# Kernel tuning notes

Hardware: AMD Instinct MI355X
Metric: run time of the kernel (lower is better)

Reference implementation:

```python
import jax, jax.numpy as jnp
import numpy as np

HEAD_SIZE = 128
BLOCK_SIZE = 2048


def setup_inputs() -> dict:
    key = jax.random.key(0)
    k1, k2 = jax.random.split(key)
    B, T, D = 8, 2048, 1024
    x = jax.random.normal(k1, (B, T, D), dtype=jnp.float32)
    # Linear(dim, 3*head_size, bias=False): weight [3*head_size, dim], applied as x @ W.T
    W_qkv = jax.random.normal(k2, (3 * HEAD_SIZE, D), dtype=jnp.float32) * (1.0 / np.sqrt(D))
    return {"x": x, "W_qkv": W_qkv}


def reference(x, W_qkv):
    B, T, D = x.shape
    qkv = jnp.einsum('btd,hd->bth', x, W_qkv)  # [B, T, 3*head_size]
    q = qkv[:, :, :HEAD_SIZE]
    k = qkv[:, :, HEAD_SIZE:2 * HEAD_SIZE]
    v = qkv[:, :, 2 * HEAD_SIZE:]
    scale = 1.0 / np.sqrt(HEAD_SIZE).astype(np.float32)
    score = jnp.einsum('bqh,bkh->bqk', q, k) * scale  # [B, T, T]
    causal = jnp.tril(jnp.ones((T, T), dtype=bool))
    score = jnp.where(causal, score, -jnp.inf)
    attn = jax.nn.softmax(score, axis=-1)
    # dropout p=0.0 (eval) -> identity
    return jnp.einsum('bqk,bkh->bqh', attn, v)  # [B, T, head_size]
```

## Files before the change

### kernel.cpp

```cpp
#include <hip/hip_runtime.h>
#include <hip/hip_bf16.h>
#include <math.h>

#define D_MODEL 1024
#define TLEN    2048

typedef __attribute__((ext_vector_type(8))) short short8;
typedef __attribute__((ext_vector_type(4))) float f32x4;

static __device__ __forceinline__ unsigned short f2bf(float f) {
    __hip_bfloat16 h = __float2bfloat16(f);
    return __builtin_bit_cast(unsigned short, h);
}
static __device__ __forceinline__ float bf2f(unsigned short u) {
    unsigned int x = ((unsigned int)u) << 16;
    return __builtin_bit_cast(float, x);
}
static __device__ __forceinline__ void lds_cp16(void* lds, const void* g) {
    __builtin_amdgcn_global_load_lds(
        (const __attribute__((address_space(1))) unsigned int*)g,
        (__attribute__((address_space(3))) unsigned int*)lds, 16, 0, 0);
}

__global__ __launch_bounds__(256) void pack_w(const float* __restrict__ W,
                                              unsigned short* __restrict__ wt) {
    const int id = blockIdx.x * 256 + threadIdx.x;
    const int h  = id >> 7;
    const int kg = id & 127;
    const int k0 = kg * 8;
    const int kt = k0 >> 6;
    const int kin = k0 & 63;
    const int np = h >> 7;
    const int hp = h & 127;
    const float4 a = *(const float4*)&W[(size_t)h * D_MODEL + k0];
    const float4 b = *(const float4*)&W[(size_t)h * D_MODEL + k0 + 4];
    short8 v;
    v[0] = (short)f2bf(a.x); v[1] = (short)f2bf(a.y);
    v[2] = (short)f2bf(a.z); v[3] = (short)f2bf(a.w);
    v[4] = (short)f2bf(b.x); v[5] = (short)f2bf(b.y);
    v[6] = (short)f2bf(b.z); v[7] = (short)f2bf(b.w);
    const size_t dst = ((size_t)(np * 16 + kt) * 128 + hp) * 64 + (kin ^ ((hp & 7) * 8));
    *(short8*)&wt[dst] = v;
}

__global__ __launch_bounds__(256, 4) void qkv_gemm(const float* __restrict__ x,
                                                   const unsigned short* __restrict__ wt,
                                                   unsigned short* __restrict__ qk,
                                                   unsigned short* __restrict__ vt) {
    __shared__ unsigned short As[64][88];
    __shared__ unsigned short Bs[128 * 64];

    const int tid  = threadIdx.x;
    const int lane = tid & 63;
    const int w    = tid >> 6;
    const int wm   = w >> 1, wn = w & 1;
    const int cc   = lane & 15, g = lane >> 4;
    const int row0 = blockIdx.x * 64;
    const int np   = blockIdx.y;

    const int xr  = tid >> 2;
    const int xc0 = (tid & 3) * 16;

    const f32x4 zero = {0.f, 0.f, 0.f, 0.f};
    f32x4 acc[2][4];
#pragma unroll
    for (int i = 0; i < 2; ++i)
#pragma unroll
        for (int j = 0; j < 4; ++j) acc[i][j] = zero;

    const float* xrow = x + (size_t)(row0 + xr) * D_MODEL + xc0;
    float4 xa[4];
#pragma unroll
    for (int i = 0; i < 4; ++i) xa[i] = *(const float4*)(xrow + i * 4);

    const unsigned short* wtile0 =
        wt + (size_t)np * 16 * 128 * 64 + (w * 4 * 1024 + lane * 16) / 2;
    unsigned short* bdst = Bs + (w * 4 * 1024) / 2;

    for (int kt = 0; kt < 16; ++kt) {
        __syncthreads();
        {
            short8 s0, s1;
            s0[0] = (short)f2bf(xa[0].x); s0[1] = (short)f2bf(xa[0].y);
            s0[2] = (short)f2bf(xa[0].z); s0[3] = (short)f2bf(xa[0].w);
            s0[4] = (short)f2bf(xa[1].x); s0[5] = (short)f2bf(xa[1].y);
            s0[6] = (short)f2bf(xa[1].z); s0[7] = (short)f2bf(xa[1].w);
            s1[0] = (short)f2bf(xa[2].x); s1[1] = (short)f2bf(xa[2].y);
            s1[2] = (short)f2bf(xa[2].z); s1[3] = (short)f2bf(xa[2].w);
            s1[4] = (short)f2bf(xa[3].x); s1[5] = (short)f2bf(xa[3].y);
            s1[6] = (short)f2bf(xa[3].z); s1[7] = (short)f2bf(xa[3].w);
            *(short8*)&As[xr][xc0]     = s0;
            *(short8*)&As[xr][xc0 + 8] = s1;
        }
        const unsigned short* wtk = wtile0 + (size_t)kt * 128 * 64;
#pragma unroll
        for (int i = 0; i < 4; ++i)
            lds_cp16(bdst + i * 512, wtk + i * 512);
        __syncthreads();

        short8 af[2][2], bf[2][4];
#pragma unroll
        for (int ks = 0; ks < 2; ++ks) {
#pragma unroll
            for (int mt = 0; mt < 2; ++mt)
                af[ks][mt] = *(const short8*)&As[wm * 32 + mt * 16 + cc][ks * 32 + g * 8];
#pragma unroll
            for (int nt = 0; nt < 4; ++nt) {
                const int h = wn * 64 + nt * 16 + cc;
                bf[ks][nt] = *(const short8*)&Bs[h * 64 + (((ks * 4 + g) ^ (h & 7)) << 3)];
            }
        }
        if (kt + 1 < 16) {
#pragma unroll
            for (int i = 0; i < 4; ++i)
                xa[i] = *(const float4*)(xrow + (kt + 1) * 64 + i * 4);
        }
        __builtin_amdgcn_s_setprio(1);
#pragma unroll
        for (int ks = 0; ks < 2; ++ks)
#pragma unroll
            for (int mt = 0; mt < 2; ++mt)
#pragma unroll
                for (int nt = 0; nt < 4; ++nt)
                    acc[mt][nt] = __builtin_amdgcn_mfma_f32_16x16x32_bf16(
                        af[ks][mt], bf[ks][nt], acc[mt][nt], 0, 0, 0);
        __builtin_amdgcn_s_setprio(0);
    }

    const int bb  = row0 >> 11;
    const int tr0 = row0 & 2047;
    const float qs = (np == 0) ? 0.08838834764831845f : 1.0f;
#pragma unroll
    for (int mt = 0; mt < 2; ++mt)
#pragma unroll
        for (int nt = 0; nt < 4; ++nt) {
            const int colp = wn * 64 + nt * 16;
            if (np < 2) {
#pragma unroll
                for (int r = 0; r < 4; ++r) {
                    const int row = row0 + wm * 32 + mt * 16 + g * 4 + r;
                    qk[(size_t)row * 256 + np * 128 + colp + cc] = f2bf(acc[mt][nt][r] * qs);
                }
            } else {
                const int d    = colp + cc;
                const int trow = tr0 + wm * 32 + mt * 16 + g * 4;
                ushort4 u;
                u.x = f2bf(acc[mt][nt][0]);
                u.y = f2bf(acc[mt][nt][1]);
                u.z = f2bf(acc[mt][nt][2]);
                u.w = f2bf(acc[mt][nt][3]);
                *(ushort4*)&vt[((size_t)(bb * 128 + d)) * TLEN + trow] = u;
            }
        }
}

__global__ __launch_bounds__(256, 3) void attn_part(const unsigned short* __restrict__ qk,
                                                    const unsigned short* __restrict__ vt,
                                                    unsigned short* __restrict__ po,
                                                    float2* __restrict__ ml) {
    __shared__ unsigned short Ks[64 * 128];
    __shared__ unsigned short Vs[128 * 64];
    __shared__ unsigned short Ps[4][16][72];

    const int tid  = threadIdx.x;
    const int lane = tid & 63;
    const int w    = tid >> 6;
    const int cc   = lane & 15, g = lane >> 4;
    const int bx   = blockIdx.x;
    const int qt   = 31 - (bx / 3);
    const int ggg  = bx % 3;
    const int b    = blockIdx.y;
    const int q0   = qt * 64;
    const int slot = (b * 32 + qt) * 3 + ggg;
    const int n    = qt + 1;
    const int cnt  = (n > ggg) ? ((n - ggg + 2) / 3) : 0;

    if (cnt == 0) {
#pragma unroll
        for (int nt = 0; nt < 8; ++nt)
#pragma unroll
            for (int r = 0; r < 4; ++r)
                po[((size_t)slot * 64 + w * 16 + g * 4 + r) * 128 + nt * 16 + cc] = 0;
        if (g == 0) ml[slot * 64 + w * 16 + cc] = make_float2(-INFINITY, 0.f);
        return;
    }

    short8 qf[4];
    {
        const unsigned short* qb =
            qk + ((size_t)(b * TLEN + q0 + w * 16 + cc)) * 256 + g * 8;
#pragma unroll
        for (int kt = 0; kt < 4; ++kt) qf[kt] = *(const short8*)(qb + kt * 32);
    }

    const f32x4 zero = {0.f, 0.f, 0.f, 0.f};
    f32x4 o[8];
#pragma unroll
    for (int nt = 0; nt < 8; ++nt) o[nt] = zero;
    float mrun = -INFINITY, lrun = 0.f;

    int koff[4], voff[2];
#pragma unroll
    for (int kt = 0; kt < 4; ++kt)
        koff[kt] = cc * 128 + (((kt * 4 + g) ^ (cc & 7)) << 3);
#pragma unroll
    for (int ks = 0; ks < 2; ++ks)
        voff[ks] = cc * 64 + (((ks * 4 + g) ^ (cc & 7)) << 3);

    const int kRow = tid >> 2;
    const int kG0  = (tid & 3) * 4;
    const int vRow = tid >> 1;
    const int vG0  = (tid & 1) * 4;
    const unsigned short* kgp = qk + ((size_t)(b * TLEN + kRow)) * 256 + 128 + kG0 * 8;
    const unsigned short* vgp = vt + ((size_t)(b * 128 + vRow)) * TLEN + vG0 * 8;

    short8 kr[4], vr[4];
#pragma unroll
    for (int i = 0; i < 4; ++i) kr[i] = *(const short8*)(kgp + (size_t)ggg * 16384 + i * 8);
#pragma unroll
    for (int i = 0; i < 4; ++i) vr[i] = *(const short8*)(vgp + ggg * 64 + i * 8);

    for (int s = 0; s < cnt; ++s) {
        const int t  = 3 * s + ggg;
        const int j0 = t * 64;
        __syncthreads();
#pragma unroll
        for (int i = 0; i < 4; ++i) {
            *(short8*)&Ks[kRow * 128 + (((kG0 + i) ^ (kRow & 7)) << 3)] = kr[i];
            *(short8*)&Vs[vRow * 64  + (((vG0 + i) ^ (vRow & 7)) << 3)] = vr[i];
        }
        __syncthreads();
        if (s + 1 < cnt) {
            const int tn = t + 3;
#pragma unroll
            for (int i = 0; i < 4; ++i) kr[i] = *(const short8*)(kgp + (size_t)tn * 16384 + i * 8);
#pragma unroll
            for (int i = 0; i < 4; ++i) vr[i] = *(const short8*)(vgp + tn * 64 + i * 8);
        }

        f32x4 st[4];
#pragma unroll
        for (int jt = 0; jt < 4; ++jt) st[jt] = zero;
        __builtin_amdgcn_s_setprio(1);
#pragma unroll
        for (int kt = 0; kt < 4; ++kt)
#pragma unroll
            for (int jt = 0; jt < 4; ++jt) {
                const short8 kf = *(const short8*)&Ks[koff[kt] + jt * 2048];
                st[jt] = __builtin_amdgcn_mfma_f32_16x16x32_bf16(kf, qf[kt], st[jt], 0, 0, 0);
            }
        __builtin_amdgcn_s_setprio(0);

        if (t == qt) {
            const int qg = q0 + w * 16 + cc;
            const int jb = j0 + 4 * g;
#pragma unroll
            for (int jt = 0; jt < 4; ++jt)
#pragma unroll
                for (int r = 0; r < 4; ++r)
                    if (jb + jt * 16 + r > qg) st[jt][r] = -INFINITY;
        }
        float pmax = -INFINITY;
#pragma unroll
        for (int jt = 0; jt < 4; ++jt) {
            const float a = fmaxf(st[jt][0], st[jt][1]);
            const float c = fmaxf(st[jt][2], st[jt][3]);
            pmax = fmaxf(pmax, fmaxf(a, c));
        }
        pmax = fmaxf(pmax, __shfl_xor(pmax, 16));
        pmax = fmaxf(pmax, __shfl_xor(pmax, 32));

        if (!__all(pmax <= mrun + 8.f)) {
            const float newm  = fmaxf(mrun, pmax);
            const float alpha = __expf(mrun - newm);
            mrun = newm;
            lrun *= alpha;
            float arow[4];
#pragma unroll
            for (int r = 0; r < 4; ++r) arow[r] = __shfl(alpha, 20 * g + r);
#pragma unroll
            for (int nt = 0; nt < 8; ++nt)
#pragma unroll
                for (int r = 0; r < 4; ++r) o[nt][r] *= arow[r];
        }

        float rs = 0.f;
#pragma unroll
        for (int jt = 0; jt < 4; ++jt) {
            const float p0 = __expf(st[jt][0] - mrun);
            const float p1 = __expf(st[jt][1] - mrun);
            const float p2 = __expf(st[jt][2] - mrun);
            const float p3 = __expf(st[jt][3] - mrun);
            rs += (p0 + p1) + (p2 + p3);
            uint2 pw;
            pw.x = (unsigned int)f2bf(p0) | ((unsigned int)f2bf(p1) << 16);
            pw.y = (unsigned int)f2bf(p2) | ((unsigned int)f2bf(p3) << 16);
            *(uint2*)&Ps[w][cc][jt * 16 + 4 * g] = pw;
        }
        rs += __shfl_xor(rs, 16);
        rs += __shfl_xor(rs, 32);
        lrun += rs;

        asm volatile("s_waitcnt lgkmcnt(0)" ::: "memory");
        __builtin_amdgcn_sched_barrier(0);

        __builtin_amdgcn_s_setprio(1);
#pragma unroll
        for (int ks = 0; ks < 2; ++ks) {
            const short8 pa = *(const short8*)&Ps[w][cc][ks * 32 + g * 8];
#pragma unroll
            for (int nt = 0; nt < 8; ++nt) {
                const short8 vf = *(const short8*)&Vs[voff[ks] + nt * 1024];
                o[nt] = __builtin_amdgcn_mfma_f32_16x16x32_bf16(pa, vf, o[nt], 0, 0, 0);
            }
        }
        __builtin_amdgcn_s_setprio(0);
    }

#pragma unroll
    for (int nt = 0; nt < 8; ++nt)
#pragma unroll
        for (int r = 0; r < 4; ++r)
            po[((size_t)slot * 64 + w * 16 + g * 4 + r) * 128 + nt * 16 + cc] =
                f2bf(o[nt][r]);
    if (g == 0) ml[slot * 64 + w * 16 + cc] = make_float2(mrun, lrun);
}

__global__ __launch_bounds__(256) void attn_merge(const unsigned short* __restrict__ po,
                                                  const float2* __restrict__ ml,
                                                  float* __restrict__ out) {
    const int bq   = blockIdx.x;
    const int row  = threadIdx.x >> 2;
    const int cs   = (threadIdx.x & 3) * 32;
    const int slot = bq * 3;

    const float2 ml0 = ml[(size_t)(slot + 0) * 64 + row];
    const float2 ml1 = ml[(size_t)(slot + 1) * 64 + row];
    const float2 ml2 = ml[(size_t)(slot + 2) * 64 + row];
    const float M  = fmaxf(fmaxf(ml0.x, ml1.x), ml2.x);
    float e0 = __expf(ml0.x - M);
    float e1 = __expf(ml1.x - M);
    float e2 = __expf(ml2.x - M);
    const float inv = 1.f / (ml0.y * e0 + ml1.y * e1 + ml2.y * e2);
    e0 *= inv; e1 *= inv; e2 *= inv;

    const unsigned short* p0 = po + ((size_t)(slot + 0) * 64 + row) * 128 + cs;
    const unsigned short* p1 = po + ((size_t)(slot + 1) * 64 + row) * 128 + cs;
    const unsigned short* p2 = po + ((size_t)(slot + 2) * 64 + row) * 128 + cs;
    float* op = out + ((size_t)bq * 64 + row) * 128 + cs;

#pragma unroll
    for (int i = 0; i < 4; ++i) {
        const short8 a = *(const short8*)(p0 + i * 8);
        const short8 b = *(const short8*)(p1 + i * 8);
        const short8 c = *(const short8*)(p2 + i * 8);
        float4 o0, o1;
        o0.x = bf2f((unsigned short)a[0]) * e0 + bf2f((unsigned short)b[0]) * e1 + bf2f((unsigned short)c[0]) * e2;
        o0.y = bf2f((unsigned short)a[1]) * e0 + bf2f((unsigned short)b[1]) * e1 + bf2f((unsigned short)c[1]) * e2;
        o0.z = bf2f((unsigned short)a[2]) * e0 + bf2f((unsigned short)b[2]) * e1 + bf2f((unsigned short)c[2]) * e2;
        o0.w = bf2f((unsigned short)a[3]) * e0 + bf2f((unsigned short)b[3]) * e1 + bf2f((unsigned short)c[3]) * e2;
        o1.x = bf2f((unsigned short)a[4]) * e0 + bf2f((unsigned short)b[4]) * e1 + bf2f((unsigned short)c[4]) * e2;
        o1.y = bf2f((unsigned short)a[5]) * e0 + bf2f((unsigned short)b[5]) * e1 + bf2f((unsigned short)c[5]) * e2;
        o1.z = bf2f((unsigned short)a[6]) * e0 + bf2f((unsigned short)b[6]) * e1 + bf2f((unsigned short)c[6]) * e2;
        o1.w = bf2f((unsigned short)a[7]) * e0 + bf2f((unsigned short)b[7]) * e1 + bf2f((unsigned short)c[7]) * e2;
        *(float4*)(op + i * 8)     = o0;
        *(float4*)(op + i * 8 + 4) = o1;
    }
}

extern "C" void kernel_launch(void* const* d_in, const int* in_sizes, int n_in,
                              void* d_out, int out_size, void* d_ws, size_t ws_size,
                              hipStream_t stream) {
    (void)in_sizes; (void)n_in; (void)out_size; (void)ws_size;
    const float* x = (const float*)d_in[0];
    const float* W = (const float*)d_in[1];
    float* out = (float*)d_out;

    unsigned short* qkbf = (unsigned short*)d_ws;
    unsigned short* vtbf = qkbf + (size_t)16384 * 256;
    unsigned short* wtbf = vtbf + (size_t)8 * 128 * 2048;
    unsigned short* pobf = wtbf + (size_t)3 * 16 * 128 * 64;
    float2*         mlf  = (float2*)(pobf + (size_t)768 * 64 * 128);

    pack_w<<<dim3(192), 256, 0, stream>>>(W, wtbf);
    qkv_gemm<<<dim3(256, 3), 256, 0, stream>>>(x, wtbf, qkbf, vtbf);
    attn_part<<<dim3(96, 8), 256, 0, stream>>>(qkbf, vtbf, pobf, mlf);
    attn_merge<<<dim3(256), 256, 0, stream>>>(pobf, mlf, out);
}
```

Baseline: 66.78 us.

## Double QKV GEMM K-tile to 128 with XOR-swizzled A tile and block remap

The QKV projection GEMM now processes K in 8 tiles of 128 instead of 16 tiles of 64. The packed weight layout and the A tile use matching XOR swizzles, so there are half as many barrier and load rounds per block. The 2D grid is flattened to 1D and remapped so the three Q/K/V column blocks of the same rows run adjacently, which should improve L2 reuse of x. The cost is more LDS and registers per block, with occupancy lowered from 4 to 3 blocks per CU.

Measured after the change: 118.7 us. 77.7% more time.

```diff
diff --git a/kernel.cpp b/kernel.cpp
--- a/kernel.cpp
+++ b/kernel.cpp
@@ -28,8 +28,8 @@
     const int h  = id >> 7;
     const int kg = id & 127;
     const int k0 = kg * 8;
-    const int kt = k0 >> 6;
-    const int kin = k0 & 63;
+    const int kt = k0 >> 7;
+    const int kin = k0 & 127;
     const int np = h >> 7;
     const int hp = h & 127;
     const float4 a = *(const float4*)&W[(size_t)h * D_MODEL + k0];
@@ -39,27 +39,33 @@
     v[2] = (short)f2bf(a.z); v[3] = (short)f2bf(a.w);
     v[4] = (short)f2bf(b.x); v[5] = (short)f2bf(b.y);
     v[6] = (short)f2bf(b.z); v[7] = (short)f2bf(b.w);
-    const size_t dst = ((size_t)(np * 16 + kt) * 128 + hp) * 64 + (kin ^ ((hp & 7) * 8));
+    const int grp = (kin >> 3) ^ (hp & 7);
+    const size_t dst = ((size_t)(np * 8 + kt) * 128 + hp) * 128 + (grp << 3);
     *(short8*)&wt[dst] = v;
 }
 
-__global__ __launch_bounds__(256, 4) void qkv_gemm(const float* __restrict__ x,
+__global__ __launch_bounds__(256, 3) void qkv_gemm(const float* __restrict__ x,
                                                    const unsigned short* __restrict__ wt,
                                                    unsigned short* __restrict__ qk,
                                                    unsigned short* __restrict__ vt) {
-    __shared__ unsigned short As[64][88];
-    __shared__ unsigned short Bs[128 * 64];
+    __shared__ unsigned short As[64 * 128];
+    __shared__ unsigned short Bs[128 * 128];
+
+    const int bid  = blockIdx.x;
+    const int u    = bid & 7;
+    const int v    = bid >> 3;
+    const int np   = v % 3;
+    const int bx   = u * 32 + v / 3;
+    const int row0 = bx * 64;
 
     const int tid  = threadIdx.x;
     const int lane = tid & 63;
     const int w    = tid >> 6;
     const int wm   = w >> 1, wn = w & 1;
     const int cc   = lane & 15, g = lane >> 4;
-    const int row0 = blockIdx.x * 64;
-    const int np   = blockIdx.y;
 
     const int xr  = tid >> 2;
-    const int xc0 = (tid & 3) * 16;
+    const int g4  = (tid & 3) * 4;
 
     const f32x4 zero = {0.f, 0.f, 0.f, 0.f};
     f32x4 acc[2][4];
@@ -68,56 +74,62 @@
 #pragma unroll
         for (int j = 0; j < 4; ++j) acc[i][j] = zero;
 
-    const float* xrow = x + (size_t)(row0 + xr) * D_MODEL + xc0;
-    float4 xa[4];
-#pragma unroll
-    for (int i = 0; i < 4; ++i) xa[i] = *(const float4*)(xrow + i * 4);
+    const float* xrow = x + (size_t)(row0 + xr) * D_MODEL + g4 * 8;
+    float4 xa[8];
+#pragma unroll
+    for (int i = 0; i < 8; ++i) xa[i] = *(const float4*)(xrow + i * 4);
 
     const unsigned short* wtile0 =
-        wt + (size_t)np * 16 * 128 * 64 + (w * 4 * 1024 + lane * 16) / 2;
-    unsigned short* bdst = Bs + (w * 4 * 1024) / 2;
-
-    for (int kt = 0; kt < 16; ++kt) {
+        wt + (size_t)np * 8 * 128 * 128 + w * 4096 + lane * 8;
+    unsigned short* bdst = Bs + w * 4096;
+
+    int awo[4];
+#pragma unroll
+    for (int i = 0; i < 4; ++i)
+        awo[i] = xr * 128 + (((g4 + i) ^ (xr & 7)) << 3);
+
+    for (int kt = 0; kt < 8; ++kt) {
         __syncthreads();
-        {
-            short8 s0, s1;
-            s0[0] = (short)f2bf(xa[0].x); s0[1] = (short)f2bf(xa[0].y);
-            s0[2] = (short)f2bf(xa[0].z); s0[3] = (short)f2bf(xa[0].w);
-            s0[4] = (short)f2bf(xa[1].x); s0[5] = (short)f2bf(xa[1].y);
-            s0[6] = (short)f2bf(xa[1].z); s0[7] = (short)f2bf(xa[1].w);
-            s1[0] = (short)f2bf(xa[2].x); s1[1] = (short)f2bf(xa[2].y);
-            s1[2] = (short)f2bf(xa[2].z); s1[3] = (short)f2bf(xa[2].w);
-            s1[4] = (short)f2bf(xa[3].x); s1[5] = (short)f2bf(xa[3].y);
-            s1[6] = (short)f2bf(xa[3].z); s1[7] = (short)f2bf(xa[3].w);
-            *(short8*)&As[xr][xc0]     = s0;
-            *(short8*)&As[xr][xc0 + 8] = s1;
-        }
-        const unsigned short* wtk = wtile0 + (size_t)kt * 128 * 64;
-#pragma unroll
-        for (int i = 0; i < 4; ++i)
+#pragma unroll
+        for (int i = 0; i < 4; ++i) {
+            const float4 a0 = xa[2 * i], a1 = xa[2 * i + 1];
+            short8 s;
+            s[0] = (short)f2bf(a0.x); s[1] = (short)f2bf(a0.y);
+            s[2] = (short)f2bf(a0.z); s[3] = (short)f2bf(a0.w);
+            s[4] = (short)f2bf(a1.x); s[5] = (short)f2bf(a1.y);
+            s[6] = (short)f2bf(a1.z); s[7] = (short)f2bf(a1.w);
+            *(short8*)&As[awo[i]] = s;
+        }
+        const unsigned short* wtk = wtile0 + (size_t)kt * 128 * 128;
+#pragma unroll
+        for (int i = 0; i < 8; ++i)
             lds_cp16(bdst + i * 512, wtk + i * 512);
         __syncthreads();
 
-        short8 af[2][2], bf[2][4];
-#pragma unroll
-        for (int ks = 0; ks < 2; ++ks) {
-#pragma unroll
-            for (int mt = 0; mt < 2; ++mt)
-                af[ks][mt] = *(const short8*)&As[wm * 32 + mt * 16 + cc][ks * 32 + g * 8];
+        short8 af[4][2], bf[4][4];
+#pragma unroll
+        for (int ks = 0; ks < 4; ++ks) {
+#pragma unroll
+            for (int mt = 0; mt < 2; ++mt) {
+                const int row = wm * 32 + mt * 16 + cc;
+                af[ks][mt] = *(const short8*)
+                    &As[row * 128 + (((ks * 4 + g) ^ (row & 7)) << 3)];
+            }
 #pragma unroll
             for (int nt = 0; nt < 4; ++nt) {
                 const int h = wn * 64 + nt * 16 + cc;
-                bf[ks][nt] = *(const short8*)&Bs[h * 64 + (((ks * 4 + g) ^ (h & 7)) << 3)];
+                bf[ks][nt] = *(const short8*)
+                    &Bs[h * 128 + (((ks * 4 + g) ^ (h & 7)) << 3)];
             }
         }
-        if (kt + 1 < 16) {
-#pragma unroll
-            for (int i = 0; i < 4; ++i)
-                xa[i] = *(const float4*)(xrow + (kt + 1) * 64 + i * 4);
+        if (kt + 1 < 8) {
+#pragma unroll
+            for (int i = 0; i < 8; ++i)
+                xa[i] = *(const float4*)(xrow + (kt + 1) * 128 + i * 4);
         }
         __builtin_amdgcn_s_setprio(1);
 #pragma unroll
-        for (int ks = 0; ks < 2; ++ks)
+        for (int ks = 0; ks < 4; ++ks)
 #pragma unroll
             for (int mt = 0; mt < 2; ++mt)
 #pragma unroll
@@ -144,12 +156,12 @@
             } else {
                 const int d    = colp + cc;
                 const int trow = tr0 + wm * 32 + mt * 16 + g * 4;
-                ushort4 u;
-                u.x = f2bf(acc[mt][nt][0]);
-                u.y = f2bf(acc[mt][nt][1]);
-                u.z = f2bf(acc[mt][nt][2]);
-                u.w = f2bf(acc[mt][nt][3]);
-                *(ushort4*)&vt[((size_t)(bb * 128 + d)) * TLEN + trow] = u;
+                ushort4 uu;
+                uu.x = f2bf(acc[mt][nt][0]);
+                uu.y = f2bf(acc[mt][nt][1]);
+                uu.z = f2bf(acc[mt][nt][2]);
+                uu.w = f2bf(acc[mt][nt][3]);
+                *(ushort4*)&vt[((size_t)(bb * 128 + d)) * TLEN + trow] = uu;
             }
         }
 }
@@ -379,11 +391,11 @@
     unsigned short* qkbf = (unsigned short*)d_ws;
     unsigned short* vtbf = qkbf + (size_t)16384 * 256;
     unsigned short* wtbf = vtbf + (size_t)8 * 128 * 2048;
-    unsigned short* pobf = wtbf + (size_t)3 * 16 * 128 * 64;
+    unsigned short* pobf = wtbf + (size_t)3 * 8 * 128 * 128;
     float2*         mlf  = (float2*)(pobf + (size_t)768 * 64 * 128);
 
     pack_w<<<dim3(192), 256, 0, stream>>>(W, wtbf);
-    qkv_gemm<<<dim3(256, 3), 256, 0, stream>>>(x, wtbf, qkbf, vtbf);
+    qkv_gemm<<<dim3(768), 256, 0, stream>>>(x, wtbf, qkbf, vtbf);
     attn_part<<<dim3(96, 8), 256, 0, stream>>>(qkbf, vtbf, pobf, mlf);
     attn_merge<<<dim3(256), 256, 0, stream>>>(pobf, mlf, out);
 }
```

## Process two 64-row query subtiles per block to reuse K/V tiles

Applied to the files above, without the earlier changes.

Each attention block now handles 128 query rows as two 64-row subtiles that share every loaded K/V tile, and the KV split grows from three to six groups so the grid stays at 96x8 blocks. This halves the K/V global and LDS traffic per query and doubles the MFMA work per LDS fetch. The cost is more registers (occupancy hint lowered to 2 blocks), twice the partial-output storage, and a six-way merge kernel. Masked rows use a clamped max to avoid NaN from fully masked subtiles.

After: 83.89 us. 1.26x slower.

```diff
diff --git a/kernel.cpp b/kernel.cpp
--- a/kernel.cpp
+++ b/kernel.cpp
@@ -154,50 +154,53 @@
         }
 }
 
-__global__ __launch_bounds__(256, 3) void attn_part(const unsigned short* __restrict__ qk,
+__global__ __launch_bounds__(256, 2) void attn_part(const unsigned short* __restrict__ qk,
                                                     const unsigned short* __restrict__ vt,
                                                     unsigned short* __restrict__ po,
                                                     float2* __restrict__ ml) {
     __shared__ unsigned short Ks[64 * 128];
     __shared__ unsigned short Vs[128 * 64];
-    __shared__ unsigned short Ps[4][16][72];
+    __shared__ unsigned short Ps[4][2][16][72];
 
     const int tid  = threadIdx.x;
     const int lane = tid & 63;
     const int w    = tid >> 6;
     const int cc   = lane & 15, g = lane >> 4;
     const int bx   = blockIdx.x;
-    const int qt   = 31 - (bx / 3);
-    const int ggg  = bx % 3;
+    const int qtb  = 15 - (bx / 6);
+    const int ggg  = bx % 6;
     const int b    = blockIdx.y;
-    const int q0   = qt * 64;
-    const int slot = (b * 32 + qt) * 3 + ggg;
-    const int n    = qt + 1;
-    const int cnt  = (n > ggg) ? ((n - ggg + 2) / 3) : 0;
+    const int q0   = qtb * 128;
+    const int slot = (b * 16 + qtb) * 6 + ggg;
+    const int n    = 2 * qtb + 2;
+    const int cnt  = (n > ggg) ? ((n - ggg + 5) / 6) : 0;
 
     if (cnt == 0) {
-#pragma unroll
-        for (int nt = 0; nt < 8; ++nt)
-#pragma unroll
-            for (int r = 0; r < 4; ++r)
-                po[((size_t)slot * 64 + w * 16 + g * 4 + r) * 128 + nt * 16 + cc] = 0;
-        if (g == 0) ml[slot * 64 + w * 16 + cc] = make_float2(-INFINITY, 0.f);
+        short8 z = {0, 0, 0, 0, 0, 0, 0, 0};
+#pragma unroll
+        for (int i = 0; i < 8; ++i)
+            *(short8*)&po[(size_t)slot * 16384 + tid * 64 + i * 8] = z;
+        if (tid < 128) ml[(size_t)slot * 128 + tid] = make_float2(-INFINITY, 0.f);
         return;
     }
 
-    short8 qf[4];
-    {
+    short8 qf[2][4];
+#pragma unroll
+    for (int su = 0; su < 2; ++su) {
         const unsigned short* qb =
-            qk + ((size_t)(b * TLEN + q0 + w * 16 + cc)) * 256 + g * 8;
-#pragma unroll
-        for (int kt = 0; kt < 4; ++kt) qf[kt] = *(const short8*)(qb + kt * 32);
+            qk + ((size_t)(b * TLEN + q0 + su * 64 + w * 16 + cc)) * 256 + g * 8;
+#pragma unroll
+        for (int kt = 0; kt < 4; ++kt) qf[su][kt] = *(const short8*)(qb + kt * 32);
     }
 
     const f32x4 zero = {0.f, 0.f, 0.f, 0.f};
-    f32x4 o[8];
-#pragma unroll
-    for (int nt = 0; nt < 8; ++nt) o[nt] = zero;
-    float mrun = -INFINITY, lrun = 0.f;
+    f32x4 o[2][8];
+#pragma unroll
+    for (int su = 0; su < 2; ++su)
+#pragma unroll
+        for (int nt = 0; nt < 8; ++nt) o[su][nt] = zero;
+    float mrun[2] = {-INFINITY, -INFINITY};
+    float lrun[2] = {0.f, 0.f};
 
     int koff[4], voff[2];
 #pragma unroll
@@ -221,7 +224,7 @@
     for (int i = 0; i < 4; ++i) vr[i] = *(const short8*)(vgp + ggg * 64 + i * 8);
 
     for (int s = 0; s < cnt; ++s) {
-        const int t  = 3 * s + ggg;
+        const int t  = ggg + 6 * s;
         const int j0 = t * 64;
         __syncthreads();
 #pragma unroll
@@ -231,75 +234,82 @@
         }
         __syncthreads();
         if (s + 1 < cnt) {
-            const int tn = t + 3;
+            const int tn = t + 6;
 #pragma unroll
             for (int i = 0; i < 4; ++i) kr[i] = *(const short8*)(kgp + (size_t)tn * 16384 + i * 8);
 #pragma unroll
             for (int i = 0; i < 4; ++i) vr[i] = *(const short8*)(vgp + tn * 64 + i * 8);
         }
 
-        f32x4 st[4];
-#pragma unroll
-        for (int jt = 0; jt < 4; ++jt) st[jt] = zero;
+        f32x4 st[2][4];
+#pragma unroll
+        for (int su = 0; su < 2; ++su)
+#pragma unroll
+            for (int jt = 0; jt < 4; ++jt) st[su][jt] = zero;
         __builtin_amdgcn_s_setprio(1);
 #pragma unroll
         for (int kt = 0; kt < 4; ++kt)
 #pragma unroll
             for (int jt = 0; jt < 4; ++jt) {
                 const short8 kf = *(const short8*)&Ks[koff[kt] + jt * 2048];
-                st[jt] = __builtin_amdgcn_mfma_f32_16x16x32_bf16(kf, qf[kt], st[jt], 0, 0, 0);
+                st[0][jt] = __builtin_amdgcn_mfma_f32_16x16x32_bf16(kf, qf[0][kt], st[0][jt], 0, 0, 0);
+                st[1][jt] = __builtin_amdgcn_mfma_f32_16x16x32_bf16(kf, qf[1][kt], st[1][jt], 0, 0, 0);
             }
         __builtin_amdgcn_s_setprio(0);
 
-        if (t == qt) {
-            const int qg = q0 + w * 16 + cc;
-            const int jb = j0 + 4 * g;
-#pragma unroll
-            for (int jt = 0; jt < 4; ++jt)
-#pragma unroll
-                for (int r = 0; r < 4; ++r)
-                    if (jb + jt * 16 + r > qg) st[jt][r] = -INFINITY;
-        }
-        float pmax = -INFINITY;
-#pragma unroll
-        for (int jt = 0; jt < 4; ++jt) {
-            const float a = fmaxf(st[jt][0], st[jt][1]);
-            const float c = fmaxf(st[jt][2], st[jt][3]);
-            pmax = fmaxf(pmax, fmaxf(a, c));
-        }
-        pmax = fmaxf(pmax, __shfl_xor(pmax, 16));
-        pmax = fmaxf(pmax, __shfl_xor(pmax, 32));
-
-        if (!__all(pmax <= mrun + 8.f)) {
-            const float newm  = fmaxf(mrun, pmax);
-            const float alpha = __expf(mrun - newm);
-            mrun = newm;
-            lrun *= alpha;
-            float arow[4];
-#pragma unroll
-            for (int r = 0; r < 4; ++r) arow[r] = __shfl(alpha, 20 * g + r);
-#pragma unroll
-            for (int nt = 0; nt < 8; ++nt)
-#pragma unroll
-                for (int r = 0; r < 4; ++r) o[nt][r] *= arow[r];
-        }
-
-        float rs = 0.f;
-#pragma unroll
-        for (int jt = 0; jt < 4; ++jt) {
-            const float p0 = __expf(st[jt][0] - mrun);
-            const float p1 = __expf(st[jt][1] - mrun);
-            const float p2 = __expf(st[jt][2] - mrun);
-            const float p3 = __expf(st[jt][3] - mrun);
-            rs += (p0 + p1) + (p2 + p3);
-            uint2 pw;
-            pw.x = (unsigned int)f2bf(p0) | ((unsigned int)f2bf(p1) << 16);
-            pw.y = (unsigned int)f2bf(p2) | ((unsigned int)f2bf(p3) << 16);
-            *(uint2*)&Ps[w][cc][jt * 16 + 4 * g] = pw;
-        }
-        rs += __shfl_xor(rs, 16);
-        rs += __shfl_xor(rs, 32);
-        lrun += rs;
+#pragma unroll
+        for (int su = 0; su < 2; ++su) {
+            const int dt = t - 2 * qtb - su;
+            if (dt >= 0) {
+                const int qg = q0 + su * 64 + w * 16 + cc;
+                const int jb = j0 + 4 * g;
+#pragma unroll
+                for (int jt = 0; jt < 4; ++jt)
+#pragma unroll
+                    for (int r = 0; r < 4; ++r)
+                        if (jb + jt * 16 + r > qg) st[su][jt][r] = -INFINITY;
+            }
+            float pmax = -INFINITY;
+#pragma unroll
+            for (int jt = 0; jt < 4; ++jt) {
+                const float a = fmaxf(st[su][jt][0], st[su][jt][1]);
+                const float c = fmaxf(st[su][jt][2], st[su][jt][3]);
+                pmax = fmaxf(pmax, fmaxf(a, c));
+            }
+            pmax = fmaxf(pmax, __shfl_xor(pmax, 16));
+            pmax = fmaxf(pmax, __shfl_xor(pmax, 32));
+
+            if (!__all(pmax <= mrun[su] + 8.f)) {
+                const float newm  = fmaxf(mrun[su], pmax);
+                const float alpha = __expf(mrun[su] - newm);
+                mrun[su] = newm;
+                lrun[su] *= alpha;
+                float arow[4];
+#pragma unroll
+                for (int r = 0; r < 4; ++r) arow[r] = __shfl(alpha, 20 * g + r);
+#pragma unroll
+                for (int nt = 0; nt < 8; ++nt)
+#pragma unroll
+                    for (int r = 0; r < 4; ++r) o[su][nt][r] *= arow[r];
+            }
+            const float meff = fmaxf(mrun[su], -1e30f);
+            float rs = 0.f;
+#pragma unroll
+            for (int jt = 0; jt < 4; ++jt) {
+                const float p0 = __expf(st[su][jt][0] - meff);
+                const float p1 = __expf(st[su][jt][1] - meff);
+                const float p2 = __expf(st[su][jt][2] - meff);
+                const float p3 = __expf(st[su][jt][3] - meff);
+                rs += (p0 + p1) + (p2 + p3);
+                uint2 pw;
+                pw.x = (unsigned int)f2bf(p0) | ((unsigned int)f2bf(p1) << 16);
+                pw.y = (unsigned int)f2bf(p2) | ((unsigned int)f2bf(p3) << 16);
+                *(uint2*)&Ps[w][su][cc][jt * 16 + 4 * g] = pw;
+            }
+            rs += __shfl_xor(rs, 16);
+            rs += __shfl_xor(rs, 32);
+            lrun[su] += rs;
+        }
 
         asm volatile("s_waitcnt lgkmcnt(0)" ::: "memory");
         __builtin_amdgcn_sched_barrier(0);
@@ -307,64 +317,71 @@
         __builtin_amdgcn_s_setprio(1);
 #pragma unroll
         for (int ks = 0; ks < 2; ++ks) {
-            const short8 pa = *(const short8*)&Ps[w][cc][ks * 32 + g * 8];
+            const short8 pa0 = *(const short8*)&Ps[w][0][cc][ks * 32 + g * 8];
+            const short8 pa1 = *(const short8*)&Ps[w][1][cc][ks * 32 + g * 8];
 #pragma unroll
             for (int nt = 0; nt < 8; ++nt) {
                 const short8 vf = *(const short8*)&Vs[voff[ks] + nt * 1024];
-                o[nt] = __builtin_amdgcn_mfma_f32_16x16x32_bf16(pa, vf, o[nt], 0, 0, 0);
+                o[0][nt] = __builtin_amdgcn_mfma_f32_16x16x32_bf16(pa0, vf, o[0][nt], 0, 0, 0);
+                o[1][nt] = __builtin_amdgcn_mfma_f32_16x16x32_bf16(pa1, vf, o[1][nt], 0, 0, 0);
             }
         }
         __builtin_amdgcn_s_setprio(0);
     }
 
 #pragma unroll
-    for (int nt = 0; nt < 8; ++nt)
-#pragma unroll
-        for (int r = 0; r < 4; ++r)
-            po[((size_t)slot * 64 + w * 16 + g * 4 + r) * 128 + nt * 16 + cc] =
-                f2bf(o[nt][r]);
-    if (g == 0) ml[slot * 64 + w * 16 + cc] = make_float2(mrun, lrun);
-}
-
-__global__ __launch_bounds__(256) void attn_merge(const unsigned short* __restrict__ po,
+    for (int su = 0; su < 2; ++su)
+#pragma unroll
+        for (int nt = 0; nt < 8; ++nt)
+#pragma unroll
+            for (int r = 0; r < 4; ++r)
+                po[((size_t)slot * 128 + su * 64 + w * 16 + g * 4 + r) * 128 + nt * 16 + cc] =
+                    f2bf(o[su][nt][r]);
+    if (g == 0) {
+        ml[(size_t)slot * 128 + w * 16 + cc]      = make_float2(mrun[0], lrun[0]);
+        ml[(size_t)slot * 128 + 64 + w * 16 + cc] = make_float2(mrun[1], lrun[1]);
+    }
+}
+
+__global__ __launch_bounds__(128) void attn_merge(const unsigned short* __restrict__ po,
                                                   const float2* __restrict__ ml,
                                                   float* __restrict__ out) {
     const int bq   = blockIdx.x;
-    const int row  = threadIdx.x >> 2;
-    const int cs   = (threadIdx.x & 3) * 32;
-    const int slot = bq * 3;
-
-    const float2 ml0 = ml[(size_t)(slot + 0) * 64 + row];
-    const float2 ml1 = ml[(size_t)(slot + 1) * 64 + row];
-    const float2 ml2 = ml[(size_t)(slot + 2) * 64 + row];
-    const float M  = fmaxf(fmaxf(ml0.x, ml1.x), ml2.x);
-    float e0 = __expf(ml0.x - M);
-    float e1 = __expf(ml1.x - M);
-    float e2 = __expf(ml2.x - M);
-    const float inv = 1.f / (ml0.y * e0 + ml1.y * e1 + ml2.y * e2);
-    e0 *= inv; e1 *= inv; e2 *= inv;
-
-    const unsigned short* p0 = po + ((size_t)(slot + 0) * 64 + row) * 128 + cs;
-    const unsigned short* p1 = po + ((size_t)(slot + 1) * 64 + row) * 128 + cs;
-    const unsigned short* p2 = po + ((size_t)(slot + 2) * 64 + row) * 128 + cs;
-    float* op = out + ((size_t)bq * 64 + row) * 128 + cs;
-
-#pragma unroll
-    for (int i = 0; i < 4; ++i) {
-        const short8 a = *(const short8*)(p0 + i * 8);
-        const short8 b = *(const short8*)(p1 + i * 8);
-        const short8 c = *(const short8*)(p2 + i * 8);
-        float4 o0, o1;
-        o0.x = bf2f((unsigned short)a[0]) * e0 + bf2f((unsigned short)b[0]) * e1 + bf2f((unsigned short)c[0]) * e2;
-        o0.y = bf2f((unsigned short)a[1]) * e0 + bf2f((unsigned short)b[1]) * e1 + bf2f((unsigned short)c[1]) * e2;
-        o0.z = bf2f((unsigned short)a[2]) * e0 + bf2f((unsigned short)b[2]) * e1 + bf2f((unsigned short)c[2]) * e2;
-        o0.w = bf2f((unsigned short)a[3]) * e0 + bf2f((unsigned short)b[3]) * e1 + bf2f((unsigned short)c[3]) * e2;
-        o1.x = bf2f((unsigned short)a[4]) * e0 + bf2f((unsigned short)b[4]) * e1 + bf2f((unsigned short)c[4]) * e2;
-        o1.y = bf2f((unsigned short)a[5]) * e0 + bf2f((unsigned short)b[5]) * e1 + bf2f((unsigned short)c[5]) * e2;
-        o1.z = bf2f((unsigned short)a[6]) * e0 + bf2f((unsigned short)b[6]) * e1 + bf2f((unsigned short)c[6]) * e2;
-        o1.w = bf2f((unsigned short)a[7]) * e0 + bf2f((unsigned short)b[7]) * e1 + bf2f((unsigned short)c[7]) * e2;
-        *(float4*)(op + i * 8)     = o0;
-        *(float4*)(op + i * 8 + 4) = o1;
+    const int cs   = blockIdx.y * 32;
+    const int row  = threadIdx.x;
+    const int slot = bq * 6;
+
+    float m[6], lv[6];
+    float M = -INFINITY;
+#pragma unroll
+    for (int i = 0; i < 6; ++i) {
+        const float2 t = ml[(size_t)(slot + i) * 128 + row];
+        m[i] = t.x; lv[i] = t.y;
+        M = fmaxf(M, m[i]);
+    }
+    float e[6];
+    float denom = 0.f;
+#pragma unroll
+    for (int i = 0; i < 6; ++i) { e[i] = __expf(m[i] - M); denom += lv[i] * e[i]; }
+    const float inv = 1.f / denom;
+#pragma unroll
+    for (int i = 0; i < 6; ++i) e[i] *= inv;
+
+    float* op = out + ((size_t)bq * 128 + row) * 128 + cs;
+#pragma unroll
+    for (int seg = 0; seg < 4; ++seg) {
+        float acc[8] = {0.f, 0.f, 0.f, 0.f, 0.f, 0.f, 0.f, 0.f};
+#pragma unroll
+        for (int i = 0; i < 6; ++i) {
+            const short8 v = *(const short8*)
+                &po[((size_t)(slot + i) * 128 + row) * 128 + cs + seg * 8];
+#pragma unroll
+            for (int k = 0; k < 8; ++k) acc[k] += bf2f((unsigned short)v[k]) * e[i];
+        }
+        float4 o0 = {acc[0], acc[1], acc[2], acc[3]};
+        float4 o1 = {acc[4], acc[5], acc[6], acc[7]};
+        *(float4*)(op + seg * 8)     = o0;
+        *(float4*)(op + seg * 8 + 4) = o1;
     }
 }
 
@@ -380,10 +397,10 @@
     unsigned short* vtbf = qkbf + (size_t)16384 * 256;
     unsigned short* wtbf = vtbf + (size_t)8 * 128 * 2048;
     unsigned short* pobf = wtbf + (size_t)3 * 16 * 128 * 64;
-    float2*         mlf  = (float2*)(pobf + (size_t)768 * 64 * 128);
+    float2*         mlf  = (float2*)(pobf + (size_t)768 * 128 * 128);
 
     pack_w<<<dim3(192), 256, 0, stream>>>(W, wtbf);
     qkv_gemm<<<dim3(256, 3), 256, 0, stream>>>(x, wtbf, qkbf, vtbf);
     attn_part<<<dim3(96, 8), 256, 0, stream>>>(qkbf, vtbf, pobf, mlf);
-    attn_merge<<<dim3(256), 256, 0, stream>>>(pobf, mlf, out);
-}
+    attn_merge<<<dim3(128, 4), 128, 0, stream>>>(pobf, mlf, out);
+}
```

## Enlarge QKV GEMM tile to 128 rows with XOR-swizzled A tile in LDS

Applied to the files above, without the earlier changes.

The QKV projection GEMM tile grows from 64 to 128 rows per block, so each wave computes a 64x64 sub-tile and each W tile loaded into LDS is reused across twice as many x rows. The A tile drops its padded layout for an XOR-swizzled one to avoid bank conflicts. The MFMA loop is split per k-step so fragment registers are smaller. The cost is half as many blocks (384 instead of 768), more accumulator registers, and occupancy lowered from 4 to 3 blocks per CU.

Result: slower. 88.16 us (+32.0%).

```diff
diff --git a/kernel.cpp b/kernel.cpp
--- a/kernel.cpp
+++ b/kernel.cpp
@@ -43,11 +43,11 @@
     *(short8*)&wt[dst] = v;
 }
 
-__global__ __launch_bounds__(256, 4) void qkv_gemm(const float* __restrict__ x,
+__global__ __launch_bounds__(256, 3) void qkv_gemm(const float* __restrict__ x,
                                                    const unsigned short* __restrict__ wt,
                                                    unsigned short* __restrict__ qk,
                                                    unsigned short* __restrict__ vt) {
-    __shared__ unsigned short As[64][88];
+    __shared__ unsigned short As[128 * 64];
     __shared__ unsigned short Bs[128 * 64];
 
     const int tid  = threadIdx.x;
@@ -55,42 +55,44 @@
     const int w    = tid >> 6;
     const int wm   = w >> 1, wn = w & 1;
     const int cc   = lane & 15, g = lane >> 4;
-    const int row0 = blockIdx.x * 64;
+    const int row0 = blockIdx.x * 128;
     const int np   = blockIdx.y;
 
-    const int xr  = tid >> 2;
-    const int xc0 = (tid & 3) * 16;
+    const int xr = tid >> 1;
+    const int gb = (tid & 1) * 4;
 
     const f32x4 zero = {0.f, 0.f, 0.f, 0.f};
-    f32x4 acc[2][4];
-#pragma unroll
-    for (int i = 0; i < 2; ++i)
+    f32x4 acc[4][4];
+#pragma unroll
+    for (int i = 0; i < 4; ++i)
 #pragma unroll
         for (int j = 0; j < 4; ++j) acc[i][j] = zero;
 
-    const float* xrow = x + (size_t)(row0 + xr) * D_MODEL + xc0;
-    float4 xa[4];
-#pragma unroll
-    for (int i = 0; i < 4; ++i) xa[i] = *(const float4*)(xrow + i * 4);
+    const float* xrow = x + (size_t)(row0 + xr) * D_MODEL + gb * 8;
+    float4 xa[8];
+#pragma unroll
+    for (int i = 0; i < 8; ++i) xa[i] = *(const float4*)(xrow + i * 4);
 
     const unsigned short* wtile0 =
-        wt + (size_t)np * 16 * 128 * 64 + (w * 4 * 1024 + lane * 16) / 2;
-    unsigned short* bdst = Bs + (w * 4 * 1024) / 2;
+        wt + (size_t)np * 16 * 128 * 64 + w * 2048 + lane * 8;
+    unsigned short* bdst = Bs + w * 2048;
+
+    int awo[4];
+#pragma unroll
+    for (int i = 0; i < 4; ++i)
+        awo[i] = xr * 64 + (((gb + i) ^ (xr & 7)) << 3);
 
     for (int kt = 0; kt < 16; ++kt) {
         __syncthreads();
-        {
-            short8 s0, s1;
-            s0[0] = (short)f2bf(xa[0].x); s0[1] = (short)f2bf(xa[0].y);
-            s0[2] = (short)f2bf(xa[0].z); s0[3] = (short)f2bf(xa[0].w);
-            s0[4] = (short)f2bf(xa[1].x); s0[5] = (short)f2bf(xa[1].y);
-            s0[6] = (short)f2bf(xa[1].z); s0[7] = (short)f2bf(xa[1].w);
-            s1[0] = (short)f2bf(xa[2].x); s1[1] = (short)f2bf(xa[2].y);
-            s1[2] = (short)f2bf(xa[2].z); s1[3] = (short)f2bf(xa[2].w);
-            s1[4] = (short)f2bf(xa[3].x); s1[5] = (short)f2bf(xa[3].y);
-            s1[6] = (short)f2bf(xa[3].z); s1[7] = (short)f2bf(xa[3].w);
-            *(short8*)&As[xr][xc0]     = s0;
-            *(short8*)&As[xr][xc0 + 8] = s1;
+#pragma unroll
+        for (int i = 0; i < 4; ++i) {
+            const float4 a0 = xa[2 * i], a1 = xa[2 * i + 1];
+            short8 s;
+            s[0] = (short)f2bf(a0.x); s[1] = (short)f2bf(a0.y);
+            s[2] = (short)f2bf(a0.z); s[3] = (short)f2bf(a0.w);
+            s[4] = (short)f2bf(a1.x); s[5] = (short)f2bf(a1.y);
+            s[6] = (short)f2bf(a1.z); s[7] = (short)f2bf(a1.w);
+            *(short8*)&As[awo[i]] = s;
         }
         const unsigned short* wtk = wtile0 + (size_t)kt * 128 * 64;
 #pragma unroll
@@ -98,52 +100,54 @@
             lds_cp16(bdst + i * 512, wtk + i * 512);
         __syncthreads();
 
-        short8 af[2][2], bf[2][4];
 #pragma unroll
         for (int ks = 0; ks < 2; ++ks) {
-#pragma unroll
-            for (int mt = 0; mt < 2; ++mt)
-                af[ks][mt] = *(const short8*)&As[wm * 32 + mt * 16 + cc][ks * 32 + g * 8];
+            short8 af[4], bf[4];
+#pragma unroll
+            for (int mt = 0; mt < 4; ++mt) {
+                const int row = wm * 64 + mt * 16 + cc;
+                af[mt] = *(const short8*)
+                    &As[row * 64 + (((ks * 4 + g) ^ (row & 7)) << 3)];
+            }
 #pragma unroll
             for (int nt = 0; nt < 4; ++nt) {
                 const int h = wn * 64 + nt * 16 + cc;
-                bf[ks][nt] = *(const short8*)&Bs[h * 64 + (((ks * 4 + g) ^ (h & 7)) << 3)];
-            }
-        }
-        if (kt + 1 < 16) {
-#pragma unroll
-            for (int i = 0; i < 4; ++i)
-                xa[i] = *(const float4*)(xrow + (kt + 1) * 64 + i * 4);
-        }
-        __builtin_amdgcn_s_setprio(1);
-#pragma unroll
-        for (int ks = 0; ks < 2; ++ks)
-#pragma unroll
-            for (int mt = 0; mt < 2; ++mt)
+                bf[nt] = *(const short8*)
+                    &Bs[h * 64 + (((ks * 4 + g) ^ (h & 7)) << 3)];
+            }
+            if (ks == 0 && kt + 1 < 16) {
+#pragma unroll
+                for (int i = 0; i < 8; ++i)
+                    xa[i] = *(const float4*)(xrow + (kt + 1) * 64 + i * 4);
+            }
+            __builtin_amdgcn_s_setprio(1);
+#pragma unroll
+            for (int mt = 0; mt < 4; ++mt)
 #pragma unroll
                 for (int nt = 0; nt < 4; ++nt)
                     acc[mt][nt] = __builtin_amdgcn_mfma_f32_16x16x32_bf16(
-                        af[ks][mt], bf[ks][nt], acc[mt][nt], 0, 0, 0);
-        __builtin_amdgcn_s_setprio(0);
+                        af[mt], bf[nt], acc[mt][nt], 0, 0, 0);
+            __builtin_amdgcn_s_setprio(0);
+        }
     }
 
     const int bb  = row0 >> 11;
     const int tr0 = row0 & 2047;
     const float qs = (np == 0) ? 0.08838834764831845f : 1.0f;
 #pragma unroll
-    for (int mt = 0; mt < 2; ++mt)
+    for (int mt = 0; mt < 4; ++mt)
 #pragma unroll
         for (int nt = 0; nt < 4; ++nt) {
             const int colp = wn * 64 + nt * 16;
             if (np < 2) {
 #pragma unroll
                 for (int r = 0; r < 4; ++r) {
-                    const int row = row0 + wm * 32 + mt * 16 + g * 4 + r;
+                    const int row = row0 + wm * 64 + mt * 16 + g * 4 + r;
                     qk[(size_t)row * 256 + np * 128 + colp + cc] = f2bf(acc[mt][nt][r] * qs);
                 }
             } else {
                 const int d    = colp + cc;
-                const int trow = tr0 + wm * 32 + mt * 16 + g * 4;
+                const int trow = tr0 + wm * 64 + mt * 16 + g * 4;
                 ushort4 u;
                 u.x = f2bf(acc[mt][nt][0]);
                 u.y = f2bf(acc[mt][nt][1]);
@@ -383,7 +387,7 @@
     float2*         mlf  = (float2*)(pobf + (size_t)768 * 64 * 128);
 
     pack_w<<<dim3(192), 256, 0, stream>>>(W, wtbf);
-    qkv_gemm<<<dim3(256, 3), 256, 0, stream>>>(x, wtbf, qkbf, vtbf);
+    qkv_gemm<<<dim3(128, 3), 256, 0, stream>>>(x, wtbf, qkbf, vtbf);
     attn_part<<<dim3(96, 8), 256, 0, stream>>>(qkbf, vtbf, pobf, mlf);
     attn_merge<<<dim3(256), 256, 0, stream>>>(pobf, mlf, out);
 }
```
